# Performance work log

Hardware: AMD Instinct MI355X
Metric: run time of the kernel (lower is better)

The kernel has to match this reference:

```python
import jax, jax.numpy as jnp
import numpy as np

N = 100_000       # nodes
E = 1_600_000     # edges
G = 128           # graphs in batch
RAW_ND, RAW_ED = 9, 3
ND, ED, H = 16, 2, 32  # node_dim, edge_dim, GAT hidden (heads=1)


def _p(key, shape, scale=0.1):
    return jax.random.normal(key, shape, dtype=jnp.float32) * scale


def setup_inputs() -> dict:
    key = jax.random.key(0)
    ks = jax.random.split(key, 32)
    inp = {
        "node_feat": jax.random.normal(ks[0], (N, RAW_ND), dtype=jnp.float32),
        "edge_index": jax.random.randint(ks[1], (2, E), 0, N, dtype=jnp.int64)
        if jax.config.jax_enable_x64 else jax.random.randint(ks[1], (2, E), 0, N).astype(jnp.int32),
        "edge_attr": jax.random.normal(ks[2], (E, RAW_ED), dtype=jnp.float32),
        "batch": jnp.sort(jax.random.randint(ks[3], (N,), 0, G)).astype(jnp.int32),
        # encoders
        "W_ne": _p(ks[4], (RAW_ND, ND)), "b_ne": jnp.zeros((ND,), jnp.float32),
        "W_ee": _p(ks[5], (RAW_ED, ED)), "b_ee": jnp.zeros((ED,), jnp.float32),
        # readout
        "W_l3": _p(ks[6], (3 * H, 1)), "b_l3": jnp.zeros((1,), jnp.float32),
    }
    dims_in = [ND, H, H]
    for i in range(3):
        k = jax.random.split(ks[7 + i], 6)
        inp[f"W{i}"] = _p(k[0], (dims_in[i], H))
        inp[f"as{i}"] = _p(k[1], (H,))
        inp[f"ad{i}"] = _p(k[2], (H,))
        inp[f"We{i}"] = _p(k[3], (ED, H))
        inp[f"ae{i}"] = _p(k[4], (H,))
        inp[f"bb{i}"] = jnp.zeros((H,), jnp.float32)
    return inp


def _segment_softmax(logits, seg, num_segments):
    m = jax.ops.segment_max(logits, seg, num_segments=num_segments)
    m = jnp.where(jnp.isfinite(m), m, 0.0)
    e = jnp.exp(logits - m[seg])
    s = jax.ops.segment_sum(e, seg, num_segments=num_segments)
    return e / (s[seg] + 1e-16)


def _gat(x, src, dst, ef, W, a_s, a_d, We, a_e, b):
    # PyG GATConv, heads=1, negative_slope=0.2
    h = x @ W                                   # [N', H]
    a_src = h @ a_s                             # [N']
    a_dst = h @ a_d
    a_edge = (ef @ We) @ a_e                    # [E']
    logits = jax.nn.leaky_relu(a_src[src] + a_dst[dst] + a_edge, 0.2)
    att = _segment_softmax(logits, dst, h.shape[0])
    out = jax.ops.segment_sum(h[src] * att[:, None], dst, num_segments=h.shape[0])
    return out + b


def reference(node_feat, edge_index, edge_attr, batch,
              W_ne, b_ne, W_ee, b_ee, W_l3, b_l3,
              W0, as0, ad0, We0, ae0, bb0,
              W1, as1, ad1, We1, ae1, bb1,
              W2, as2, ad2, We2, ae2, bb2):
    n = node_feat.shape[0]
    x = node_feat @ W_ne + b_ne                 # NodeEncoder -> [N,16]
    ef = edge_attr @ W_ee + b_ee                # EdgeEncoder -> [E,2]
    # add_self_loops=True with fill_value='mean' (PyG default when edge_dim set)
    loop = jnp.arange(n, dtype=edge_index.dtype)
    src = jnp.concatenate([edge_index[0], loop])
    dst = jnp.concatenate([edge_index[1], loop])
    ef_fill = jnp.broadcast_to(ef.mean(axis=0), (n, ef.shape[1]))
    ef_aug = jnp.concatenate([ef, ef_fill], axis=0)
    x1 = _gat(x, src, dst, ef_aug, W0, as0, ad0, We0, ae0, bb0)
    x2 = _gat(x1, src, dst, ef_aug, W1, as1, ad1, We1, ae1, bb1)
    x3 = _gat(x2, src, dst, ef_aug, W2, as2, ad2, We2, ae2, bb2)
    x_cat = jnp.concatenate([x1, x2, x3], axis=1)  # [N, 96]
    sums = jax.ops.segment_sum(x_cat, batch, num_segments=G)
    cnt = jax.ops.segment_sum(jnp.ones((n,), x_cat.dtype), batch, num_segments=G)
    pooled = sums / jnp.maximum(cnt, 1.0)[:, None]   # global mean pool [G,96]
    return pooled @ W_l3 + b_l3                      # [G,1]
```

## Files before the change

### kernel.cpp

```cpp
#include <hip/hip_runtime.h>
#include <hip/hip_fp16.h>


#define NBUCK_SHIFT 8
#define NBUCK_MAX 512
#define CAP 6144

__global__ void k_pre(const float4* __restrict__ ea4, const float* __restrict__ Wee,
                      const float* __restrict__ bee, float2* __restrict__ partial,
                      const int* __restrict__ ei1, int* __restrict__ bucket_cnt,
                      const int* __restrict__ batch, int* __restrict__ bounds,
                      const float* __restrict__ Wne, const float* __restrict__ bne,
                      const float* __restrict__ W0, float* __restrict__ wf,
                      int n, int e, int ep, int nbCS, int nbH) {
    int b = blockIdx.x, t = threadIdx.x;
    if (b < nbCS) {
        int tid = b * 256 + t;
        int e4 = e >> 2;
        float s0 = 0.f, s1 = 0.f;
        if (tid < e4) {
            float4 q0 = ea4[tid * 3], q1 = ea4[tid * 3 + 1], q2 = ea4[tid * 3 + 2];
            float a = q0.x + q0.w + q1.z + q2.y;
            float b2 = q0.y + q1.x + q1.w + q2.z;
            float c = q0.z + q1.y + q2.x + q2.w;
            s0 = a * Wee[0] + b2 * Wee[2] + c * Wee[4] + 4.f * bee[0];
            s1 = a * Wee[1] + b2 * Wee[3] + c * Wee[5] + 4.f * bee[1];
        }
#pragma unroll
        for (int off = 32; off > 0; off >>= 1) {
            s0 += __shfl_xor(s0, off, 64);
            s1 += __shfl_xor(s1, off, 64);
        }
        if ((t & 63) == 0)
            partial[(b << 2) + (t >> 6)] = make_float2(s0, s1);
        return;
    }
    b -= nbCS;
    if (b < nbH) {
        __shared__ int lh[NBUCK_MAX];
        lh[t] = 0; lh[t + 256] = 0;
        __syncthreads();
        int base = b * 4096;
#pragma unroll
        for (int i = 0; i < 16; ++i) {
            int gid = base + i * 256 + t;
            if (gid < ep) {
                int d = (gid < e) ? ei1[gid] : gid - e;
                atomicAdd(&lh[d >> NBUCK_SHIFT], 1);
            }
        }
        __syncthreads();
        if (lh[t]) atomicAdd(&bucket_cnt[t], lh[t]);
        if (lh[t + 256]) atomicAdd(&bucket_cnt[t + 256], lh[t + 256]);
        return;
    }
    for (int i = t; i < 288; i += 256) {
        int m = i >> 5, j = i & 31;
        float a = 0.f;
        for (int k = 0; k < 16; ++k) a += Wne[m * 16 + k] * W0[k * 32 + j];
        wf[i] = a;
    }
    if (t < 32) {
        float a = 0.f;
        for (int k = 0; k < 16; ++k) a += bne[k] * W0[k * 32 + t];
        wf[288 + t] = a;
    }
    for (int g = t; g <= 128; g += 256) {
        if (g == 128) { bounds[128] = n; continue; }
        int lo = 0, hi = n;
        while (lo < hi) {
            int mid = (lo + hi) >> 1;
            if (batch[mid] < g) lo = mid + 1; else hi = mid;
        }
        bounds[g] = lo;
    }
}

__global__ void k_hproj0(const float* __restrict__ nf, const float* __restrict__ wf,
                         const float* __restrict__ as_, const float* __restrict__ ad_,
                         unsigned int* __restrict__ h2, float* __restrict__ asrc,
                         float* __restrict__ adst, int n) {
    int node = blockIdx.x * 8 + (threadIdx.x >> 5);
    int j = threadIdx.x & 31;
    if (node >= n) return;
    const float* xr = nf + node * 9;
    float acc = wf[288 + j];
#pragma unroll
    for (int m = 0; m < 9; ++m) acc += xr[m] * wf[m * 32 + j];
    float accp = __shfl_down(acc, 1, 32);
    if ((j & 1) == 0) {
        __half2 hh = __floats2half2_rn(acc, accp);
        h2[(size_t)node * 16 + (j >> 1)] = *reinterpret_cast<unsigned int*>(&hh);
    }
    float r1 = acc * as_[j], r2 = acc * ad_[j];
#pragma unroll
    for (int off = 16; off > 0; off >>= 1) {
        r1 += __shfl_xor(r1, off, 32);
        r2 += __shfl_xor(r2, off, 32);
    }
    if (j == 0) { asrc[node] = r1; adst[node] = r2; }
}

__global__ void k_hproj(const float* __restrict__ x, const float* __restrict__ W,
                        const float* __restrict__ as_, const float* __restrict__ ad_,
                        unsigned int* __restrict__ h2, float* __restrict__ asrc,
                        float* __restrict__ adst, int n) {
    __shared__ float sW[1024];
    for (int i = threadIdx.x; i < 1024; i += 256) sW[i] = W[i];
    __syncthreads();
    int node = blockIdx.x * 8 + (threadIdx.x >> 5);
    int j = threadIdx.x & 31;
    if (node >= n) return;
    const float* xr = x + (size_t)node * 32;
    float acc = 0.f;
#pragma unroll
    for (int k = 0; k < 32; ++k) acc += xr[k] * sW[k * 32 + j];
    float accp = __shfl_down(acc, 1, 32);
    if ((j & 1) == 0) {
        __half2 hh = __floats2half2_rn(acc, accp);
        h2[(size_t)node * 16 + (j >> 1)] = *reinterpret_cast<unsigned int*>(&hh);
    }
    float r1 = acc * as_[j], r2 = acc * ad_[j];
#pragma unroll
    for (int off = 16; off > 0; off >>= 1) {
        r1 += __shfl_xor(r1, off, 32);
        r2 += __shfl_xor(r2, off, 32);
    }
    if (j == 0) { asrc[node] = r1; adst[node] = r2; }
}

__global__ void __launch_bounds__(512)
k_mid(const float* __restrict__ We0, const float* __restrict__ ae0,
      const float* __restrict__ We1, const float* __restrict__ ae1,
      const float* __restrict__ We2, const float* __restrict__ ae2,
      const float2* __restrict__ partial, int nw, float einv,
      float* __restrict__ consts,
      const int* __restrict__ bucket_cnt, int* __restrict__ bucket_base,
      int* __restrict__ bcursor, int nbuck, int ep, int* __restrict__ rp, int n) {
    int t = threadIdx.x;
    if (blockIdx.x == 0) {
        __shared__ float r0[512], r1[512];
        float m0 = 0.f, m1 = 0.f;
        for (int i = t; i < nw; i += 512) {
            float2 v = partial[i];
            m0 += v.x; m1 += v.y;
        }
        r0[t] = m0; r1[t] = m1;
        __syncthreads();
        for (int o = 256; o > 0; o >>= 1) {
            if (t < o) { r0[t] += r0[t + o]; r1[t] += r1[t + o]; }
            __syncthreads();
        }
        if (t == 0) {
            consts[12] = r0[0] * einv;
            consts[13] = r1[0] * einv;
            const float* We[3] = {We0, We1, We2};
            const float* ae[3] = {ae0, ae1, ae2};
            for (int l = 0; l < 3; ++l) {
                float c0 = 0.f, c1 = 0.f;
                for (int j = 0; j < 32; ++j) {
                    c0 += We[l][j] * ae[l][j];
                    c1 += We[l][32 + j] * ae[l][j];
                }
                consts[l * 2 + 0] = c0;
                consts[l * 2 + 1] = c1;
            }
        }
    } else {
        __shared__ int s[512];
        int v = (t < nbuck) ? bucket_cnt[t] : 0;
        s[t] = v;
        __syncthreads();
        for (int o = 1; o < 512; o <<= 1) {
            int x = (t >= o) ? s[t - o] : 0;
            __syncthreads();
            s[t] += x;
            __syncthreads();
        }
        int ex = s[t] - v;
        if (t < nbuck) { bucket_base[t] = ex; bcursor[t] = ex; }
        if (t == 0) { bucket_base[nbuck] = ep; rp[n] = ep; }
    }
}

__global__ void k_binB(const int* __restrict__ ei0, const int* __restrict__ ei1,
                       const float* __restrict__ ea, const float* __restrict__ We,
                       const float* __restrict__ be, const float* __restrict__ consts,
                       int* __restrict__ bcursor, uint2* __restrict__ st, int e, int ep) {
    __shared__ int lh[NBUCK_MAX], lcur[NBUCK_MAX];
    int t = threadIdx.x;
    lh[t] = 0; lh[t + 256] = 0;
    __syncthreads();
    int base = blockIdx.x * 4096;
    unsigned int sd[16], fh[16];
    int bk[16];
    float w00 = We[0], w10 = We[2], w20 = We[4];
    float w01 = We[1], w11 = We[3], w21 = We[5];
    float b0 = be[0], b1 = be[1];
#pragma unroll
    for (int i = 0; i < 16; ++i) {
        int gid = base + i * 256 + t;
        bk[i] = -1;
        if (gid < ep) {
            int s, d; float f0, f1;
            if (gid < e) {
                s = ei0[gid]; d = ei1[gid];
                const float* r = ea + (size_t)gid * 3;
                float a0 = r[0], a1 = r[1], a2 = r[2];
                f0 = a0 * w00 + a1 * w10 + a2 * w20 + b0;
                f1 = a0 * w01 + a1 * w11 + a2 * w21 + b1;
            } else {
                s = d = gid - e;
                f0 = consts[12]; f1 = consts[13];
            }
            bk[i] = d >> NBUCK_SHIFT;
            sd[i] = ((unsigned int)s << NBUCK_SHIFT) | (unsigned int)(d & 255);
            __half2 hh = __floats2half2_rn(f0, f1);
            fh[i] = *reinterpret_cast<unsigned int*>(&hh);
            atomicAdd(&lh[bk[i]], 1);
        }
    }
    __syncthreads();
    if (lh[t] > 0) lcur[t] = atomicAdd(&bcursor[t], lh[t]);
    if (lh[t + 256] > 0) lcur[t + 256] = atomicAdd(&bcursor[t + 256], lh[t + 256]);
    __syncthreads();
#pragma unroll
    for (int i = 0; i < 16; ++i) {
        if (bk[i] >= 0) {
            int pos = atomicAdd(&lcur[bk[i]], 1);
            st[pos] = make_uint2(sd[i], fh[i]);
        }
    }
}

__global__ void __launch_bounds__(512)
k_binC(const uint2* __restrict__ st, const int* __restrict__ bucket_base,
       int* __restrict__ rp, uint2* __restrict__ rec, int n) {
    __shared__ int nh[256], ns[256];
    __shared__ uint2 rs[CAP];
    int k = blockIdx.x, t = threadIdx.x;
    int s0 = bucket_base[k], s1 = bucket_base[k + 1];
    int cnt = s1 - s0;
    uint2 lv[12];
    if (t < 256) nh[t] = 0;
    __syncthreads();
#pragma unroll
    for (int u = 0; u < 12; ++u) {
        int i = s0 + u * 512 + t;
        if (i < s1) {
            uint2 v = st[i];
            lv[u] = v;
            atomicAdd(&nh[v.x & 255], 1);
        }
    }
    __syncthreads();
    if (t < 256) ns[t] = nh[t];
    __syncthreads();
    for (int o = 1; o < 256; o <<= 1) {
        int add = 0;
        if (t < 256 && t >= o) add = ns[t - o];
        __syncthreads();
        if (t < 256) ns[t] += add;
        __syncthreads();
    }
    int node0 = k << NBUCK_SHIFT;
    if (t < 256) {
        int startl = ns[t] - nh[t];
        if (node0 + t < n) rp[node0 + t] = s0 + startl;
        nh[t] = startl;
    }
    __syncthreads();
#pragma unroll
    for (int u = 0; u < 12; ++u) {
        int i = s0 + u * 512 + t;
        if (i < s1) {
            uint2 v = lv[u];
            int pos = atomicAdd(&nh[v.x & 255], 1);
            uint2 r = make_uint2(v.x >> NBUCK_SHIFT, v.y);
            if (pos < CAP) rs[pos] = r;
            else rec[s0 + pos] = r;
        }
    }
    __syncthreads();
    int m = cnt < CAP ? cnt : CAP;
    for (int i = t; i < m; i += 512)
        rec[s0 + i] = rs[i];
}

__device__ __forceinline__ float h2_get(const unsigned int* __restrict__ h2,
                                        int s, int word, bool hi) {
    unsigned int hw = h2[(size_t)s * 16 + word];
    __half2 hh = *reinterpret_cast<__half2*>(&hw);
    return hi ? __high2float(hh) : __low2float(hh);
}

template <bool STORE_X>
__global__ void k_agg(const int* __restrict__ rp, const uint2* __restrict__ rec,
                      const float* __restrict__ asrc, const float* __restrict__ adst,
                      const float* __restrict__ consts, const unsigned int* __restrict__ h2,
                      const float* __restrict__ bb, float* __restrict__ xout,
                      const float* __restrict__ wl3, float* __restrict__ vout,
                      int n, int layer) {
    int node = blockIdx.x * 8 + (threadIdx.x >> 5);
    int j = threadIdx.x & 31;
    if (node >= n) return;
    float c0 = consts[layer * 2], c1 = consts[layer * 2 + 1];
    int r0 = rp[node], r1 = rp[node + 1];
    float adn = adst[node];
    int word = j >> 1;
    bool hi = (j & 1) != 0;
    float acc = 0.f, psum = 0.f;
    for (int c = r0; c < r1; c += 32) {
        int i = c + j;
        float pe = 0.f; int s = 0;
        if (i < r1) {
            unsigned long long rv = __builtin_nontemporal_load(
                reinterpret_cast<const unsigned long long*>(rec + i));
            s = (int)(unsigned int)(rv & 0xffffffffull);
            unsigned int fv = (unsigned int)(rv >> 32);
            __half2 hh = *reinterpret_cast<__half2*>(&fv);
            float lg = asrc[s] + adn + __low2float(hh) * c0 + __high2float(hh) * c1;
            lg = lg > 0.f ? lg : 0.2f * lg;
            pe = __expf(lg);
        }
        psum += pe;
        int cnt = min(32, r1 - c);
        int t = 0;
        for (; t + 8 <= cnt; t += 8) {
            int s0 = __shfl(s, t, 32),     s1 = __shfl(s, t + 1, 32);
            int s2 = __shfl(s, t + 2, 32), s3 = __shfl(s, t + 3, 32);
            int s4 = __shfl(s, t + 4, 32), s5 = __shfl(s, t + 5, 32);
            int s6 = __shfl(s, t + 6, 32), s7 = __shfl(s, t + 7, 32);
            float p0 = __shfl(pe, t, 32),     p1 = __shfl(pe, t + 1, 32);
            float p2 = __shfl(pe, t + 2, 32), p3 = __shfl(pe, t + 3, 32);
            float p4 = __shfl(pe, t + 4, 32), p5 = __shfl(pe, t + 5, 32);
            float p6 = __shfl(pe, t + 6, 32), p7 = __shfl(pe, t + 7, 32);
            float h0 = h2_get(h2, s0, word, hi);
            float h1 = h2_get(h2, s1, word, hi);
            float h2v = h2_get(h2, s2, word, hi);
            float h3 = h2_get(h2, s3, word, hi);
            float h4 = h2_get(h2, s4, word, hi);
            float h5 = h2_get(h2, s5, word, hi);
            float h6 = h2_get(h2, s6, word, hi);
            float h7 = h2_get(h2, s7, word, hi);
            acc += p0 * h0; acc += p1 * h1; acc += p2 * h2v; acc += p3 * h3;
            acc += p4 * h4; acc += p5 * h5; acc += p6 * h6; acc += p7 * h7;
        }
        for (; t + 4 <= cnt; t += 4) {
            int s0 = __shfl(s, t, 32),     s1 = __shfl(s, t + 1, 32);
            int s2 = __shfl(s, t + 2, 32), s3 = __shfl(s, t + 3, 32);
            float p0 = __shfl(pe, t, 32),     p1 = __shfl(pe, t + 1, 32);
            float p2 = __shfl(pe, t + 2, 32), p3 = __shfl(pe, t + 3, 32);
            float h0 = h2_get(h2, s0, word, hi);
            float h1 = h2_get(h2, s1, word, hi);
            float h2v = h2_get(h2, s2, word, hi);
            float h3 = h2_get(h2, s3, word, hi);
            acc += p0 * h0; acc += p1 * h1; acc += p2 * h2v; acc += p3 * h3;
        }
        for (; t < cnt; ++t) {
            int st2 = __shfl(s, t, 32);
            float pt = __shfl(pe, t, 32);
            acc += pt * h2_get(h2, st2, word, hi);
        }
    }
#pragma unroll
    for (int off = 16; off > 0; off >>= 1) psum += __shfl_xor(psum, off, 32);
    float res = acc / (psum + 1e-16f) + bb[j];
    if (STORE_X) xout[(size_t)node * 32 + j] = res;
    float v = res * wl3[j];
#pragma unroll
    for (int off = 16; off > 0; off >>= 1) v += __shfl_xor(v, off, 32);
    if (j == 0) vout[node] = v;
}

__global__ void k_dotv(const float* __restrict__ v0, const float* __restrict__ v1,
                       const float* __restrict__ v2, const int* __restrict__ bounds,
                       const float* __restrict__ bl3, float* __restrict__ out) {
    __shared__ float red[256];
    int g = blockIdx.x, t = threadIdx.x;
    int s0 = bounds[g], s1 = bounds[g + 1];
    float acc = 0.f;
    for (int i = s0 + t; i < s1; i += 256) acc += v0[i] + v1[i] + v2[i];
    red[t] = acc;
    __syncthreads();
    for (int o = 128; o > 0; o >>= 1) {
        if (t < o) red[t] += red[t + o];
        __syncthreads();
    }
    if (t == 0) {
        float c = (float)(s1 - s0);
        if (c < 1.f) c = 1.f;
        out[g] = red[0] / c + bl3[0];
    }
}

extern "C" void kernel_launch(void* const* d_in, const int* in_sizes, int n_in,
                              void* d_out, int out_size, void* d_ws, size_t ws_size,
                              hipStream_t stream) {
    (void)n_in; (void)out_size; (void)ws_size;
    const float* nf    = (const float*)d_in[0];
    const int*   ei    = (const int*)d_in[1];
    const float* ea    = (const float*)d_in[2];
    const int*   batch = (const int*)d_in[3];
    const float* W_ne  = (const float*)d_in[4];
    const float* b_ne  = (const float*)d_in[5];
    const float* W_ee  = (const float*)d_in[6];
    const float* b_ee  = (const float*)d_in[7];
    const float* W_l3  = (const float*)d_in[8];
    const float* b_l3  = (const float*)d_in[9];
    const float *Wl[3], *asl[3], *adl[3], *Wel[3], *ael[3], *bbl[3];
    for (int l = 0; l < 3; ++l) {
        Wl[l]  = (const float*)d_in[10 + 6 * l];
        asl[l] = (const float*)d_in[11 + 6 * l];
        adl[l] = (const float*)d_in[12 + 6 * l];
        Wel[l] = (const float*)d_in[13 + 6 * l];
        ael[l] = (const float*)d_in[14 + 6 * l];
        bbl[l] = (const float*)d_in[15 + 6 * l];
    }

    const int n  = in_sizes[3];
    const int e  = in_sizes[2] / 3;
    const int ep = e + n;
    const int* ei0 = ei;
    const int* ei1 = ei + e;
    const int nbuck = (n + 255) >> NBUCK_SHIFT;

    char* w = (char*)d_ws;
    size_t off = 0;
    auto alloc = [&](size_t b) { size_t o = off; off = (off + b + 255) & ~(size_t)255; return o; };
    float*        x1      = (float*)(w + alloc((size_t)n * 32 * 4));
    float*        x2      = (float*)(w + alloc((size_t)n * 32 * 4));
    unsigned int* h2a     = (unsigned int*)(w + alloc((size_t)n * 16 * 4));
    unsigned int* h2b     = (unsigned int*)(w + alloc((size_t)n * 16 * 4));
    float*        asrcA   = (float*)(w + alloc((size_t)n * 4));
    float*        adstA   = (float*)(w + alloc((size_t)n * 4));
    float*        asrcB   = (float*)(w + alloc((size_t)n * 4));
    float*        adstB   = (float*)(w + alloc((size_t)n * 4));
    float*        v0      = (float*)(w + alloc((size_t)n * 4));
    float*        v1      = (float*)(w + alloc((size_t)n * 4));
    float*        v2      = (float*)(w + alloc((size_t)n * 4));
    uint2*        st      = (uint2*)(w + alloc((size_t)ep * 8));
    uint2*        rec     = (uint2*)(w + alloc((size_t)ep * 8));
    int*          rp      = (int*)(w + alloc((size_t)(n + 1) * 4));
    int*          bcnt    = (int*)(w + alloc(NBUCK_MAX * 4));
    int*          bbase   = (int*)(w + alloc((NBUCK_MAX + 1) * 4));
    int*          bcur    = (int*)(w + alloc(NBUCK_MAX * 4));
    float2*       partial = (float2*)(w + alloc((size_t)8192 * 8));
    float*        consts  = (float*)(w + alloc(256));
    int*          bounds  = (int*)(w + alloc(129 * 4));
    float*        wfbuf   = (float*)(w + alloc(320 * 4));

    hipMemsetAsync(bcnt, 0, NBUCK_MAX * 4, stream);

    int e4   = e >> 2;
    int nbCS = (e4 + 255) / 256;
    int nbH  = (ep + 4095) / 4096;
    int nw   = nbCS * 4;
    int nbN  = (n + 7) / 8;

    k_pre<<<nbCS + nbH + 1, 256, 0, stream>>>(
        (const float4*)ea, W_ee, b_ee, partial, ei1, bcnt, batch, bounds,
        W_ne, b_ne, Wl[0], wfbuf, n, e, ep, nbCS, nbH);
    k_hproj0<<<nbN, 256, 0, stream>>>(nf, wfbuf, asl[0], adl[0],
                                      h2a, asrcA, adstA, n);
    k_mid<<<2, 512, 0, stream>>>(Wel[0], ael[0], Wel[1], ael[1], Wel[2], ael[2],
                                 partial, nw, 1.0f / (float)e, consts,
                                 bcnt, bbase, bcur, nbuck, ep, rp, n);
    k_binB<<<nbH, 256, 0, stream>>>(ei0, ei1, ea, W_ee, b_ee, consts, bcur, st, e, ep);
    k_binC<<<nbuck, 512, 0, stream>>>(st, bbase, rp, rec, n);

    k_agg<true><<<nbN, 256, 0, stream>>>(rp, rec, asrcA, adstA, consts, h2a,
                                         bbl[0], x1, W_l3 + 0, v0, n, 0);
    k_hproj<<<nbN, 256, 0, stream>>>(x1, Wl[1], asl[1], adl[1], h2b, asrcB, adstB, n);
    k_agg<true><<<nbN, 256, 0, stream>>>(rp, rec, asrcB, adstB, consts, h2b,
                                         bbl[1], x2, W_l3 + 32, v1, n, 1);
    k_hproj<<<nbN, 256, 0, stream>>>(x2, Wl[2], asl[2], adl[2], h2a, asrcA, adstA, n);
    k_agg<false><<<nbN, 256, 0, stream>>>(rp, rec, asrcA, adstA, consts, h2a,
                                          bbl[2], nullptr, W_l3 + 64, v2, n, 2);
    k_dotv<<<128, 256, 0, stream>>>(v0, v1, v2, bounds, b_l3, (float*)d_out);
}
```

Baseline: 348.3 us.

## Fuse edge-feature mean into binning, flag self-loops, store hidden features in fp16

```diff
diff --git a/kernel.cpp b/kernel.cpp
--- a/kernel.cpp
+++ b/kernel.cpp
@@ -5,37 +5,14 @@
 #define NBUCK_SHIFT 8
 #define NBUCK_MAX 512
 #define CAP 6144
-
-__global__ void k_pre(const float4* __restrict__ ea4, const float* __restrict__ Wee,
-                      const float* __restrict__ bee, float2* __restrict__ partial,
-                      const int* __restrict__ ei1, int* __restrict__ bucket_cnt,
+#define SLF_BIT 0x00800000u
+
+__global__ void k_pre(const int* __restrict__ ei1, int* __restrict__ bucket_cnt,
                       const int* __restrict__ batch, int* __restrict__ bounds,
                       const float* __restrict__ Wne, const float* __restrict__ bne,
                       const float* __restrict__ W0, float* __restrict__ wf,
-                      int n, int e, int ep, int nbCS, int nbH) {
+                      int n, int e, int ep, int nbH) {
     int b = blockIdx.x, t = threadIdx.x;
-    if (b < nbCS) {
-        int tid = b * 256 + t;
-        int e4 = e >> 2;
-        float s0 = 0.f, s1 = 0.f;
-        if (tid < e4) {
-            float4 q0 = ea4[tid * 3], q1 = ea4[tid * 3 + 1], q2 = ea4[tid * 3 + 2];
-            float a = q0.x + q0.w + q1.z + q2.y;
-            float b2 = q0.y + q1.x + q1.w + q2.z;
-            float c = q0.z + q1.y + q2.x + q2.w;
-            s0 = a * Wee[0] + b2 * Wee[2] + c * Wee[4] + 4.f * bee[0];
-            s1 = a * Wee[1] + b2 * Wee[3] + c * Wee[5] + 4.f * bee[1];
-        }
-#pragma unroll
-        for (int off = 32; off > 0; off >>= 1) {
-            s0 += __shfl_xor(s0, off, 64);
-            s1 += __shfl_xor(s1, off, 64);
-        }
-        if ((t & 63) == 0)
-            partial[(b << 2) + (t >> 6)] = make_float2(s0, s1);
-        return;
-    }
-    b -= nbCS;
     if (b < nbH) {
         __shared__ int lh[NBUCK_MAX];
         lh[t] = 0; lh[t + 256] = 0;
@@ -101,7 +78,12 @@
     if (j == 0) { asrc[node] = r1; adst[node] = r2; }
 }
 
-__global__ void k_hproj(const float* __restrict__ x, const float* __restrict__ W,
+__device__ __forceinline__ float2 h2f2u(unsigned int hw) {
+    __half2 hh = *reinterpret_cast<__half2*>(&hw);
+    return make_float2(__low2float(hh), __high2float(hh));
+}
+
+__global__ void k_hproj(const unsigned int* __restrict__ xh, const float* __restrict__ W,
                         const float* __restrict__ as_, const float* __restrict__ ad_,
                         unsigned int* __restrict__ h2, float* __restrict__ asrc,
                         float* __restrict__ adst, int n) {
@@ -111,10 +93,13 @@
     int node = blockIdx.x * 8 + (threadIdx.x >> 5);
     int j = threadIdx.x & 31;
     if (node >= n) return;
-    const float* xr = x + (size_t)node * 32;
+    const unsigned int* xr = xh + (size_t)node * 16;
     float acc = 0.f;
 #pragma unroll
-    for (int k = 0; k < 32; ++k) acc += xr[k] * sW[k * 32 + j];
+    for (int w = 0; w < 16; ++w) {
+        float2 f = h2f2u(xr[w]);
+        acc += f.x * sW[(2 * w) * 32 + j] + f.y * sW[(2 * w + 1) * 32 + j];
+    }
     float accp = __shfl_down(acc, 1, 32);
     if ((j & 1) == 0) {
         __half2 hh = __floats2half2_rn(acc, accp);
@@ -130,15 +115,96 @@
 }
 
 __global__ void __launch_bounds__(512)
-k_mid(const float* __restrict__ We0, const float* __restrict__ ae0,
-      const float* __restrict__ We1, const float* __restrict__ ae1,
-      const float* __restrict__ We2, const float* __restrict__ ae2,
-      const float2* __restrict__ partial, int nw, float einv,
-      float* __restrict__ consts,
-      const int* __restrict__ bucket_cnt, int* __restrict__ bucket_base,
-      int* __restrict__ bcursor, int nbuck, int ep, int* __restrict__ rp, int n) {
+k_scan(const int* __restrict__ bucket_cnt, int* __restrict__ bucket_base,
+       int* __restrict__ bcursor, int nbuck, int ep, int* __restrict__ rp, int n) {
+    __shared__ int s[512];
     int t = threadIdx.x;
-    if (blockIdx.x == 0) {
+    int v = (t < nbuck) ? bucket_cnt[t] : 0;
+    s[t] = v;
+    __syncthreads();
+    for (int o = 1; o < 512; o <<= 1) {
+        int x = (t >= o) ? s[t - o] : 0;
+        __syncthreads();
+        s[t] += x;
+        __syncthreads();
+    }
+    int ex = s[t] - v;
+    if (t < nbuck) { bucket_base[t] = ex; bcursor[t] = ex; }
+    if (t == 0) { bucket_base[nbuck] = ep; rp[n] = ep; }
+}
+
+__global__ void k_binB(const int* __restrict__ ei0, const int* __restrict__ ei1,
+                       const float* __restrict__ ea, const float* __restrict__ We,
+                       const float* __restrict__ be, int* __restrict__ bcursor,
+                       uint2* __restrict__ st, float2* __restrict__ partial,
+                       int e, int ep) {
+    __shared__ int lh[NBUCK_MAX], lcur[NBUCK_MAX];
+    int t = threadIdx.x;
+    lh[t] = 0; lh[t + 256] = 0;
+    __syncthreads();
+    int base = blockIdx.x * 4096;
+    unsigned int sd[16], fh[16];
+    int bk[16];
+    float w00 = We[0], w10 = We[2], w20 = We[4];
+    float w01 = We[1], w11 = We[3], w21 = We[5];
+    float b0 = be[0], b1 = be[1];
+    float cs0 = 0.f, cs1 = 0.f;
+#pragma unroll
+    for (int i = 0; i < 16; ++i) {
+        int gid = base + i * 256 + t;
+        bk[i] = -1;
+        if (gid < ep) {
+            int s, d;
+            if (gid < e) {
+                s = ei0[gid]; d = ei1[gid];
+                const float* r = ea + (size_t)gid * 3;
+                float a0 = r[0], a1 = r[1], a2 = r[2];
+                float f0 = a0 * w00 + a1 * w10 + a2 * w20 + b0;
+                float f1 = a0 * w01 + a1 * w11 + a2 * w21 + b1;
+                cs0 += f0; cs1 += f1;
+                sd[i] = ((unsigned int)s << NBUCK_SHIFT) | (unsigned int)(d & 255);
+                __half2 hh = __floats2half2_rn(f0, f1);
+                fh[i] = *reinterpret_cast<unsigned int*>(&hh);
+            } else {
+                s = d = gid - e;
+                sd[i] = 0x80000000u | ((unsigned int)s << NBUCK_SHIFT)
+                      | (unsigned int)(d & 255);
+                fh[i] = 0;
+            }
+            bk[i] = d >> NBUCK_SHIFT;
+            atomicAdd(&lh[bk[i]], 1);
+        }
+    }
+#pragma unroll
+    for (int off = 32; off > 0; off >>= 1) {
+        cs0 += __shfl_xor(cs0, off, 64);
+        cs1 += __shfl_xor(cs1, off, 64);
+    }
+    if ((t & 63) == 0)
+        partial[(blockIdx.x << 2) + (t >> 6)] = make_float2(cs0, cs1);
+    __syncthreads();
+    if (lh[t] > 0) lcur[t] = atomicAdd(&bcursor[t], lh[t]);
+    if (lh[t + 256] > 0) lcur[t + 256] = atomicAdd(&bcursor[t + 256], lh[t + 256]);
+    __syncthreads();
+#pragma unroll
+    for (int i = 0; i < 16; ++i) {
+        if (bk[i] >= 0) {
+            int pos = atomicAdd(&lcur[bk[i]], 1);
+            st[pos] = make_uint2(sd[i], fh[i]);
+        }
+    }
+}
+
+__global__ void __launch_bounds__(512)
+k_binC(const uint2* __restrict__ st, const int* __restrict__ bucket_base,
+       int* __restrict__ rp, uint2* __restrict__ rec, int n, int nbuck,
+       const float* __restrict__ We0, const float* __restrict__ ae0,
+       const float* __restrict__ We1, const float* __restrict__ ae1,
+       const float* __restrict__ We2, const float* __restrict__ ae2,
+       const float2* __restrict__ partial, int nw, float einv,
+       float* __restrict__ consts) {
+    int k = blockIdx.x, t = threadIdx.x;
+    if (k == nbuck) {
         __shared__ float r0[512], r1[512];
         float m0 = 0.f, m1 = 0.f;
         for (int i = t; i < nw; i += 512) {
@@ -152,8 +218,7 @@
             __syncthreads();
         }
         if (t == 0) {
-            consts[12] = r0[0] * einv;
-            consts[13] = r1[0] * einv;
+            float fm0 = r0[0] * einv, fm1 = r1[0] * einv;
             const float* We[3] = {We0, We1, We2};
             const float* ae[3] = {ae0, ae1, ae2};
             for (int l = 0; l < 3; ++l) {
@@ -164,81 +229,13 @@
                 }
                 consts[l * 2 + 0] = c0;
                 consts[l * 2 + 1] = c1;
+                consts[6 + l] = fm0 * c0 + fm1 * c1;
             }
         }
-    } else {
-        __shared__ int s[512];
-        int v = (t < nbuck) ? bucket_cnt[t] : 0;
-        s[t] = v;
-        __syncthreads();
-        for (int o = 1; o < 512; o <<= 1) {
-            int x = (t >= o) ? s[t - o] : 0;
-            __syncthreads();
-            s[t] += x;
-            __syncthreads();
-        }
-        int ex = s[t] - v;
-        if (t < nbuck) { bucket_base[t] = ex; bcursor[t] = ex; }
-        if (t == 0) { bucket_base[nbuck] = ep; rp[n] = ep; }
-    }
-}
-
-__global__ void k_binB(const int* __restrict__ ei0, const int* __restrict__ ei1,
-                       const float* __restrict__ ea, const float* __restrict__ We,
-                       const float* __restrict__ be, const float* __restrict__ consts,
-                       int* __restrict__ bcursor, uint2* __restrict__ st, int e, int ep) {
-    __shared__ int lh[NBUCK_MAX], lcur[NBUCK_MAX];
-    int t = threadIdx.x;
-    lh[t] = 0; lh[t + 256] = 0;
-    __syncthreads();
-    int base = blockIdx.x * 4096;
-    unsigned int sd[16], fh[16];
-    int bk[16];
-    float w00 = We[0], w10 = We[2], w20 = We[4];
-    float w01 = We[1], w11 = We[3], w21 = We[5];
-    float b0 = be[0], b1 = be[1];
-#pragma unroll
-    for (int i = 0; i < 16; ++i) {
-        int gid = base + i * 256 + t;
-        bk[i] = -1;
-        if (gid < ep) {
-            int s, d; float f0, f1;
-            if (gid < e) {
-                s = ei0[gid]; d = ei1[gid];
-                const float* r = ea + (size_t)gid * 3;
-                float a0 = r[0], a1 = r[1], a2 = r[2];
-                f0 = a0 * w00 + a1 * w10 + a2 * w20 + b0;
-                f1 = a0 * w01 + a1 * w11 + a2 * w21 + b1;
-            } else {
-                s = d = gid - e;
-                f0 = consts[12]; f1 = consts[13];
-            }
-            bk[i] = d >> NBUCK_SHIFT;
-            sd[i] = ((unsigned int)s << NBUCK_SHIFT) | (unsigned int)(d & 255);
-            __half2 hh = __floats2half2_rn(f0, f1);
-            fh[i] = *reinterpret_cast<unsigned int*>(&hh);
-            atomicAdd(&lh[bk[i]], 1);
-        }
-    }
-    __syncthreads();
-    if (lh[t] > 0) lcur[t] = atomicAdd(&bcursor[t], lh[t]);
-    if (lh[t + 256] > 0) lcur[t + 256] = atomicAdd(&bcursor[t + 256], lh[t + 256]);
-    __syncthreads();
-#pragma unroll
-    for (int i = 0; i < 16; ++i) {
-        if (bk[i] >= 0) {
-            int pos = atomicAdd(&lcur[bk[i]], 1);
-            st[pos] = make_uint2(sd[i], fh[i]);
-        }
-    }
-}
-
-__global__ void __launch_bounds__(512)
-k_binC(const uint2* __restrict__ st, const int* __restrict__ bucket_base,
-       int* __restrict__ rp, uint2* __restrict__ rec, int n) {
+        return;
+    }
     __shared__ int nh[256], ns[256];
     __shared__ uint2 rs[CAP];
-    int k = blockIdx.x, t = threadIdx.x;
     int s0 = bucket_base[k], s1 = bucket_base[k + 1];
     int cnt = s1 - s0;
     uint2 lv[12];
@@ -298,13 +295,14 @@
 __global__ void k_agg(const int* __restrict__ rp, const uint2* __restrict__ rec,
                       const float* __restrict__ asrc, const float* __restrict__ adst,
                       const float* __restrict__ consts, const unsigned int* __restrict__ h2,
-                      const float* __restrict__ bb, float* __restrict__ xout,
+                      const float* __restrict__ bb, unsigned int* __restrict__ xout,
                       const float* __restrict__ wl3, float* __restrict__ vout,
                       int n, int layer) {
     int node = blockIdx.x * 8 + (threadIdx.x >> 5);
     int j = threadIdx.x & 31;
     if (node >= n) return;
     float c0 = consts[layer * 2], c1 = consts[layer * 2 + 1];
+    float loopc = consts[6 + layer];
     int r0 = rp[node], r1 = rp[node + 1];
     float adn = adst[node];
     int word = j >> 1;
@@ -316,10 +314,13 @@
         if (i < r1) {
             unsigned long long rv = __builtin_nontemporal_load(
                 reinterpret_cast<const unsigned long long*>(rec + i));
-            s = (int)(unsigned int)(rv & 0xffffffffull);
+            unsigned int sx = (unsigned int)(rv & 0xffffffffull);
+            s = (int)(sx & 0x7fffffu);
             unsigned int fv = (unsigned int)(rv >> 32);
             __half2 hh = *reinterpret_cast<__half2*>(&fv);
-            float lg = asrc[s] + adn + __low2float(hh) * c0 + __high2float(hh) * c1;
+            float ae = (sx & SLF_BIT) ? loopc
+                     : (__low2float(hh) * c0 + __high2float(hh) * c1);
+            float lg = asrc[s] + adn + ae;
             lg = lg > 0.f ? lg : 0.2f * lg;
             pe = __expf(lg);
         }
@@ -366,7 +367,13 @@
 #pragma unroll
     for (int off = 16; off > 0; off >>= 1) psum += __shfl_xor(psum, off, 32);
     float res = acc / (psum + 1e-16f) + bb[j];
-    if (STORE_X) xout[(size_t)node * 32 + j] = res;
+    if (STORE_X) {
+        float resp = __shfl_down(res, 1, 32);
+        if ((j & 1) == 0) {
+            __half2 hh = __floats2half2_rn(res, resp);
+            xout[(size_t)node * 16 + (j >> 1)] = *reinterpret_cast<unsigned int*>(&hh);
+        }
+    }
     float v = res * wl3[j];
 #pragma unroll
     for (int off = 16; off > 0; off >>= 1) v += __shfl_xor(v, off, 32);
@@ -428,8 +435,8 @@
     char* w = (char*)d_ws;
     size_t off = 0;
     auto alloc = [&](size_t b) { size_t o = off; off = (off + b + 255) & ~(size_t)255; return o; };
-    float*        x1      = (float*)(w + alloc((size_t)n * 32 * 4));
-    float*        x2      = (float*)(w + alloc((size_t)n * 32 * 4));
+    unsigned int* x1h     = (unsigned int*)(w + alloc((size_t)n * 16 * 4));
+    unsigned int* x2h     = (unsigned int*)(w + alloc((size_t)n * 16 * 4));
     unsigned int* h2a     = (unsigned int*)(w + alloc((size_t)n * 16 * 4));
     unsigned int* h2b     = (unsigned int*)(w + alloc((size_t)n * 16 * 4));
     float*        asrcA   = (float*)(w + alloc((size_t)n * 4));
@@ -452,29 +459,28 @@
 
     hipMemsetAsync(bcnt, 0, NBUCK_MAX * 4, stream);
 
-    int e4   = e >> 2;
-    int nbCS = (e4 + 255) / 256;
-    int nbH  = (ep + 4095) / 4096;
-    int nw   = nbCS * 4;
-    int nbN  = (n + 7) / 8;
-
-    k_pre<<<nbCS + nbH + 1, 256, 0, stream>>>(
-        (const float4*)ea, W_ee, b_ee, partial, ei1, bcnt, batch, bounds,
-        W_ne, b_ne, Wl[0], wfbuf, n, e, ep, nbCS, nbH);
+    int nbH = (ep + 4095) / 4096;
+    int nw  = nbH * 4;
+    int nbN = (n + 7) / 8;
+
+    k_pre<<<nbH + 1, 256, 0, stream>>>(ei1, bcnt, batch, bounds,
+                                       W_ne, b_ne, Wl[0], wfbuf, n, e, ep, nbH);
     k_hproj0<<<nbN, 256, 0, stream>>>(nf, wfbuf, asl[0], adl[0],
                                       h2a, asrcA, adstA, n);
-    k_mid<<<2, 512, 0, stream>>>(Wel[0], ael[0], Wel[1], ael[1], Wel[2], ael[2],
-                                 partial, nw, 1.0f / (float)e, consts,
-                                 bcnt, bbase, bcur, nbuck, ep, rp, n);
-    k_binB<<<nbH, 256, 0, stream>>>(ei0, ei1, ea, W_ee, b_ee, consts, bcur, st, e, ep);
-    k_binC<<<nbuck, 512, 0, stream>>>(st, bbase, rp, rec, n);
+    k_scan<<<1, 512, 0, stream>>>(bcnt, bbase, bcur, nbuck, ep, rp, n);
+    k_binB<<<nbH, 256, 0, stream>>>(ei0, ei1, ea, W_ee, b_ee, bcur, st,
+                                    partial, e, ep);
+    k_binC<<<nbuck + 1, 512, 0, stream>>>(st, bbase, rp, rec, n, nbuck,
+                                          Wel[0], ael[0], Wel[1], ael[1],
+                                          Wel[2], ael[2], partial, nw,
+                                          1.0f / (float)e, consts);
 
     k_agg<true><<<nbN, 256, 0, stream>>>(rp, rec, asrcA, adstA, consts, h2a,
-                                         bbl[0], x1, W_l3 + 0, v0, n, 0);
-    k_hproj<<<nbN, 256, 0, stream>>>(x1, Wl[1], asl[1], adl[1], h2b, asrcB, adstB, n);
+                                         bbl[0], x1h, W_l3 + 0, v0, n, 0);
+    k_hproj<<<nbN, 256, 0, stream>>>(x1h, Wl[1], asl[1], adl[1], h2b, asrcB, adstB, n);
     k_agg<true><<<nbN, 256, 0, stream>>>(rp, rec, asrcB, adstB, consts, h2b,
-                                         bbl[1], x2, W_l3 + 32, v1, n, 1);
-    k_hproj<<<nbN, 256, 0, stream>>>(x2, Wl[2], asl[2], adl[2], h2a, asrcA, adstA, n);
+                                         bbl[1], x2h, W_l3 + 32, v1, n, 1);
+    k_hproj<<<nbN, 256, 0, stream>>>(x2h, Wl[2], asl[2], adl[2], h2a, asrcA, adstA, n);
     k_agg<false><<<nbN, 256, 0, stream>>>(rp, rec, asrcA, adstA, consts, h2a,
                                           bbl[2], nullptr, W_l3 + 64, v2, n, 2);
     k_dotv<<<128, 256, 0, stream>>>(v0, v1, v2, bounds, b_l3, (float*)d_out);
```

New measurement: 340.9 us (median of 2 runs). -2.1%, faster.
